# Performance work log

Hardware: AMD Instinct MI355X
Metric: run time of the kernel (lower is better)

The kernel has to match this reference:

```python
import jax, jax.numpy as jnp
import numpy as np

N = 100000   # nodes
E = 1600000  # edges
IN, H1, H2, OUT = 512, 64, 16, 40


def setup_inputs() -> dict:
    key = jax.random.key(0)
    ks = jax.random.split(key, 8)
    x = jax.random.normal(ks[0], (N, IN), jnp.float32)
    edge_index = jax.random.randint(ks[1], (2, E), 0, N, dtype=jnp.int64)

    def glorot(k, i, o):
        s = np.sqrt(6.0 / (i + o)).astype(np.float32)
        return jax.random.uniform(k, (i, o), jnp.float32, -s, s)

    return dict(
        x=x, edge_index=edge_index,
        W1=glorot(ks[2], IN, H1), b1=jnp.zeros((H1,), jnp.float32),
        W2=glorot(ks[3], H1, H2), b2=jnp.zeros((H2,), jnp.float32),
        W3=glorot(ks[4], H2, OUT), b3=jnp.zeros((OUT,), jnp.float32),
    )


def _gcn_conv(x, src, dst, W, b):
    # PyG GCNConv: x' = D^{-1/2} (A + I) D^{-1/2} (x W) + b
    h = x @ W                                   # [N, F_out]
    n = x.shape[0]
    deg = jnp.zeros((n,), h.dtype).at[dst].add(1.0) + 1.0   # self-loop adds 1
    dinv = jax.lax.rsqrt(deg)                   # deg >= 1 always
    norm = dinv[src] * dinv[dst]                # [E]
    msg = h[src] * norm[:, None]                # gather + scale  [E, F_out]
    out = jnp.zeros_like(h).at[dst].add(msg)    # scatter-add to targets
    out = out + h * (dinv * dinv)[:, None]      # self-loop contribution
    return out + b


def reference(x, edge_index, W1, b1, W2, b2, W3, b3):
    src, dst = edge_index[0], edge_index[1]
    h = jax.nn.relu(_gcn_conv(x, src, dst, W1, b1))
    # dropout(p=0.2, training=False) -> identity
    h = jax.nn.relu(_gcn_conv(h, src, dst, W2, b2))
    h = _gcn_conv(h, src, dst, W3, b3)
    return jax.nn.log_softmax(h, axis=-1)
```

## Files before the change

kernel.cpp:

```cpp
#include <hip/hip_runtime.h>
#include <cstdint>
#include <cstddef>

#define NNODES 100000
#define NEDGES 1600000
#define NWIN 100
#define WIN_NODES 1000
#define WCAP 17408
#define WSTR 16

#define GM_ROWS 128
#define APAD 72
#define GEMM_BLOCKS ((NNODES + GM_ROWS - 1) / GM_ROWS)
#define BUCKET_BLOCKS 512
#define BCHUNK ((NEDGES + BUCKET_BLOCKS - 1) / BUCKET_BLOCKS)
#define MEGA_BLOCKS (GEMM_BLOCKS + BUCKET_BLOCKS)

typedef __attribute__((ext_vector_type(8))) short bf16x8;
typedef __attribute__((ext_vector_type(4))) float f32x4;

__device__ inline unsigned short f2bf(float f) {
    union { float f; unsigned u; } v; v.f = f;
    unsigned r = v.u + 0x7FFFu + ((v.u >> 16) & 1u);
    return (unsigned short)(r >> 16);
}
__device__ inline void bfpair(unsigned u, float& lo, float& hi) {
    union { unsigned x; float f; } a, b;
    a.x = u << 16; b.x = u & 0xffff0000u;
    lo = a.f; hi = b.f;
}


__global__ __launch_bounds__(256) void convW(const float* __restrict__ W,
                                             unsigned short* __restrict__ Wt,
                                             int* __restrict__ wcur) {
    if (blockIdx.x == 0 && threadIdx.x < NWIN) wcur[threadIdx.x * WSTR] = 0;
    int i = blockIdx.x * 256 + threadIdx.x;
    if (i < 512 * 64) {
        int k = i >> 6, n = i & 63;
        Wt[n * 512 + k] = f2bf(W[i]);
    }
}


__global__ __launch_bounds__(256) void mega_gemm_bucket(
        const float* __restrict__ A,
        const unsigned short* __restrict__ Wt,
        unsigned short* __restrict__ Hs,
        const int* __restrict__ src, const int* __restrict__ dst,
        unsigned* __restrict__ stage,
        int* __restrict__ wcur, int M, int E) {
    __shared__ __align__(16) unsigned char smem[4 * 32 * APAD * 2];

    long long b = blockIdx.x;
    int g0 = (int)((b * GEMM_BLOCKS) / MEGA_BLOCKS);
    int g1 = (int)(((b + 1) * GEMM_BLOCKS) / MEGA_BLOCKS);

    if (g1 > g0) {
        typedef unsigned short Slice[32][APAD];
        Slice* As = (Slice*)smem;
        const int tid = threadIdx.x;
        const int wv = tid >> 6;
        const int lane = tid & 63;
        const int lm = lane & 15;
        const int lk = (lane >> 4) * 8;
        const int lr4 = lane >> 4;
        const int lc4 = lane & 15;
        const int bm = g0 * GM_ROWS + wv * 32;

        f32x4 acc[2][4];
#pragma unroll
        for (int i = 0; i < 2; i++)
#pragma unroll
            for (int j = 0; j < 4; j++) acc[i][j] = (f32x4){0.f, 0.f, 0.f, 0.f};

        for (int k0 = 0; k0 < 512; k0 += 64) {
#pragma unroll
            for (int p = 0; p < 8; p++) {
                int rl = p * 4 + lr4;
                int row = bm + rl;
                float4 v;
                if (row < M) v = *(const float4*)&A[(size_t)row * 512 + k0 + lc4 * 4];
                else         v = make_float4(0.f, 0.f, 0.f, 0.f);
                unsigned lo, hi;
                asm("v_cvt_pk_bf16_f32 %0, %1, %2" : "=v"(lo) : "v"(v.x), "v"(v.y));
                asm("v_cvt_pk_bf16_f32 %0, %1, %2" : "=v"(hi) : "v"(v.z), "v"(v.w));
                uint2 u; u.x = lo; u.y = hi;
                *(uint2*)&As[wv][rl][lc4 * 4] = u;
            }
            bf16x8 af[2][2];
#pragma unroll
            for (int rf = 0; rf < 2; rf++)
#pragma unroll
                for (int kf = 0; kf < 2; kf++)
                    af[rf][kf] = *(const bf16x8*)&As[wv][rf * 16 + lm][kf * 32 + lk];
            bf16x8 bf[4][2];
#pragma unroll
            for (int cf = 0; cf < 4; cf++)
#pragma unroll
                for (int kf = 0; kf < 2; kf++)
                    bf[cf][kf] = *(const bf16x8*)&Wt[(size_t)(cf * 16 + lm) * 512 + k0 + kf * 32 + lk];

            __builtin_amdgcn_s_setprio(1);
#pragma unroll
            for (int kf = 0; kf < 2; kf++)
#pragma unroll
                for (int rf = 0; rf < 2; rf++)
#pragma unroll
                    for (int cf = 0; cf < 4; cf++)
                        acc[rf][cf] = __builtin_amdgcn_mfma_f32_16x16x32_bf16(
                            af[rf][kf], bf[cf][kf], acc[rf][cf], 0, 0, 0);
            __builtin_amdgcn_s_setprio(0);
        }

#pragma unroll
        for (int rf = 0; rf < 2; rf++) {
#pragma unroll
            for (int j = 0; j < 4; j++) {
                int row = bm + rf * 16 + (lane >> 4) * 4 + j;
                if (row < M) {
#pragma unroll
                    for (int cf = 0; cf < 4; cf++)
                        Hs[(size_t)row * 64 + cf * 16 + lm] = f2bf(acc[rf][cf][j]);
                }
            }
        }
    } else {
        int bi = (int)(b - g0);
        int* cnt  = (int*)smem;
        int* lcur = cnt + NWIN;
        const int tid = threadIdx.x;
        int e0 = bi * BCHUNK;
        int e1 = e0 + BCHUNK; if (e1 > E) e1 = E;

        for (int i = tid; i < NWIN; i += 256) cnt[i] = 0;
        __syncthreads();
        for (int e = e0 + tid; e < e1; e += 256)
            atomicAdd(&cnt[dst[e] / WIN_NODES], 1);
        __syncthreads();
        for (int i = tid; i < NWIN; i += 256)
            lcur[i] = atomicAdd(&wcur[i * WSTR], cnt[i]);
        __syncthreads();
        for (int e = e0 + tid; e < e1; e += 256) {
            int d = dst[e], s = src[e];
            int w = d / WIN_NODES;
            int pos = atomicAdd(&lcur[w], 1);
            if (pos < WCAP)
                stage[(size_t)w * WCAP + pos] =
                    ((unsigned)(d - w * WIN_NODES) << 17) | (unsigned)s;
        }
    }
}


__global__ __launch_bounds__(256) void csr_window(
        const unsigned* __restrict__ stage,
        const int* __restrict__ wcur,
        int* __restrict__ rowstart,
        float* __restrict__ dinv,
        int* __restrict__ csr) {
    __shared__ int cnt[WIN_NODES];
    __shared__ int red[256];
    const int w = blockIdx.x;
    const int t = threadIdx.x;
    const int wb = w * WIN_NODES;
    const size_t sb = (size_t)w * WCAP;

    int v = (t < w) ? min(wcur[t * WSTR], WCAP) : 0;
    red[t] = v;
    __syncthreads();
#pragma unroll
    for (int off = 128; off > 0; off >>= 1) {
        if (t < off) red[t] += red[t + off];
        __syncthreads();
    }
    int woff = red[0];
    int n_w = min(wcur[w * WSTR], WCAP);
    __syncthreads();

    for (int i = t; i < WIN_NODES; i += 256) cnt[i] = 0;
    __syncthreads();
    for (int i = t; i < n_w; i += 256)
        atomicAdd(&cnt[stage[sb + i] >> 17], 1);
    __syncthreads();

    int c0 = 0, c1 = 0, c2 = 0, c3 = 0, psum = 0;
    if (t < 250) {
        c0 = cnt[4 * t]; c1 = cnt[4 * t + 1]; c2 = cnt[4 * t + 2]; c3 = cnt[4 * t + 3];
        psum = c0 + c1 + c2 + c3;
    }
    red[t] = psum;
    __syncthreads();
#pragma unroll
    for (int off = 1; off < 256; off <<= 1) {
        int tv = (t >= off) ? red[t - off] : 0;
        __syncthreads();
        red[t] += tv;
        __syncthreads();
    }
    int excl = red[t] - psum;
    if (t < 250) {
        int running = woff + excl;
        int idx = 4 * t;
        rowstart[wb + idx] = running; dinv[wb + idx] = rsqrtf((float)c0 + 1.f);
        cnt[idx] = running; running += c0;
        rowstart[wb + idx + 1] = running; dinv[wb + idx + 1] = rsqrtf((float)c1 + 1.f);
        cnt[idx + 1] = running; running += c1;
        rowstart[wb + idx + 2] = running; dinv[wb + idx + 2] = rsqrtf((float)c2 + 1.f);
        cnt[idx + 2] = running; running += c2;
        rowstart[wb + idx + 3] = running; dinv[wb + idx + 3] = rsqrtf((float)c3 + 1.f);
        cnt[idx + 3] = running;
    }
    if (w == NWIN - 1 && t == 0) rowstart[NNODES] = woff + n_w;
    __syncthreads();

    for (int i = t; i < n_w; i += 256) {
        unsigned p = stage[sb + i];
        int dl = (int)(p >> 17);
        int s  = (int)(p & 0x1FFFFu);
        int pos = atomicAdd(&cnt[dl], 1);
        csr[pos] = s;
    }
}


__global__ __launch_bounds__(256) void gather64_l2(
        const int* __restrict__ rowstart, const int* __restrict__ csr,
        const float* __restrict__ dinv,
        const unsigned short* __restrict__ Hs1,
        const float* __restrict__ b1,
        const float* __restrict__ W2,
        unsigned short* __restrict__ Hs2,
        int M) {
    __shared__ float Ws2[64 * 16];
    __shared__ float b1s[64];
    __shared__ float srow[8][64];
    for (int i = threadIdx.x; i < 64 * 16; i += 256) Ws2[i] = W2[i];
    if (threadIdx.x < 64) b1s[threadIdx.x] = b1[threadIdx.x];
    __syncthreads();

    const int r = threadIdx.x >> 5;
    const int lf = threadIdx.x & 31;
    const int row = blockIdx.x * 8 + r;
    const bool rok = (row < M);

    float v0 = 0.f, v1 = 0.f;
    if (rok) {
        const unsigned* H32 = (const unsigned*)Hs1;
        int e0 = rowstart[row], e1 = rowstart[row + 1];
        float dd = dinv[row];
        float acc0, acc1;
        bfpair(H32[(size_t)row * 32 + lf], acc0, acc1);
        acc0 *= dd; acc1 *= dd;
        int e = e0;
        for (; e + 3 < e1; e += 4) {
            int s0 = csr[e], s1 = csr[e + 1], s2 = csr[e + 2], s3 = csr[e + 3];
            float w0 = dinv[s0], w1 = dinv[s1], w2 = dinv[s2], w3 = dinv[s3];
            unsigned u0 = H32[(size_t)s0 * 32 + lf];
            unsigned u1 = H32[(size_t)s1 * 32 + lf];
            unsigned u2 = H32[(size_t)s2 * 32 + lf];
            unsigned u3 = H32[(size_t)s3 * 32 + lf];
            float a, b;
            bfpair(u0, a, b); acc0 += w0 * a; acc1 += w0 * b;
            bfpair(u1, a, b); acc0 += w1 * a; acc1 += w1 * b;
            bfpair(u2, a, b); acc0 += w2 * a; acc1 += w2 * b;
            bfpair(u3, a, b); acc0 += w3 * a; acc1 += w3 * b;
        }
        for (; e < e1; e++) {
            int s0 = csr[e];
            float w0 = dinv[s0];
            unsigned u = H32[(size_t)s0 * 32 + lf];
            float a, b;
            bfpair(u, a, b); acc0 += w0 * a; acc1 += w0 * b;
        }
        v0 = fmaxf(acc0 * dd + b1s[2 * lf], 0.f);
        v1 = fmaxf(acc1 * dd + b1s[2 * lf + 1], 0.f);
    }
    float2 t2; t2.x = v0; t2.y = v1;
    *(float2*)&srow[r][2 * lf] = t2;
    __syncthreads();

    if (rok && lf < 16) {
        float acc = 0.f;
#pragma unroll
        for (int k4 = 0; k4 < 16; k4++) {
            float4 s4 = *(const float4*)&srow[r][k4 * 4];
            acc += s4.x * Ws2[(k4 * 4 + 0) * 16 + lf];
            acc += s4.y * Ws2[(k4 * 4 + 1) * 16 + lf];
            acc += s4.z * Ws2[(k4 * 4 + 2) * 16 + lf];
            acc += s4.w * Ws2[(k4 * 4 + 3) * 16 + lf];
        }
        acc *= dinv[row];
        float hi = __shfl_down(acc, 1, 64);
        if ((lf & 1) == 0) {
            unsigned p = (unsigned)f2bf(acc) | ((unsigned)f2bf(hi) << 16);
            ((unsigned*)Hs2)[(size_t)row * 8 + (lf >> 1)] = p;
        }
    }
}


template <int F, bool RELU, bool SCALEOUT, bool HASBIAS, bool OUTBF>
__global__ __launch_bounds__(256) void gather_bf(
        const int* __restrict__ rowstart,
        const int* __restrict__ csr,
        const float* __restrict__ dinv,
        const unsigned short* __restrict__ Hs,
        const float* __restrict__ bias,
        void* __restrict__ outp,
        int M) {
    constexpr int LANES = F / 2;
    constexpr int GP = 256 / LANES;
    int row = blockIdx.x * GP + threadIdx.x / LANES;
    int lf = threadIdx.x % LANES;
    if (row >= M) return;

    const unsigned* H32 = (const unsigned*)Hs;
    const size_t LP = F / 2;

    int e0 = rowstart[row], e1 = rowstart[row + 1];
    float acc0, acc1;
    bfpair(H32[(size_t)row * LP + lf], acc0, acc1);

    int e = e0;
    for (; e + 3 < e1; e += 4) {
        int s0 = csr[e], s1 = csr[e + 1], s2 = csr[e + 2], s3 = csr[e + 3];
        unsigned u0 = H32[(size_t)s0 * LP + lf];
        unsigned u1 = H32[(size_t)s1 * LP + lf];
        unsigned u2 = H32[(size_t)s2 * LP + lf];
        unsigned u3 = H32[(size_t)s3 * LP + lf];
        float a, b;
        bfpair(u0, a, b); acc0 += a; acc1 += b;
        bfpair(u1, a, b); acc0 += a; acc1 += b;
        bfpair(u2, a, b); acc0 += a; acc1 += b;
        bfpair(u3, a, b); acc0 += a; acc1 += b;
    }
    for (; e < e1; e++) {
        unsigned u = H32[(size_t)csr[e] * LP + lf];
        float a, b;
        bfpair(u, a, b); acc0 += a; acc1 += b;
    }

    float dd = dinv[row];
    float v0 = acc0 * dd, v1 = acc1 * dd;
    if (HASBIAS) { v0 += bias[2 * lf]; v1 += bias[2 * lf + 1]; }
    if (RELU) { v0 = fmaxf(v0, 0.f); v1 = fmaxf(v1, 0.f); }
    if (SCALEOUT) { v0 *= dd; v1 *= dd; }
    if (OUTBF) {
        unsigned p = (unsigned)f2bf(v0) | ((unsigned)f2bf(v1) << 16);
        ((unsigned*)outp)[(size_t)row * LP + lf] = p;
    } else {
        float2 t; t.x = v0; t.y = v1;
        ((float2*)outp)[(size_t)row * LP + lf] = t;
    }
}


#define SRP 20

__global__ __launch_bounds__(256) void gather16_final(
        const int* __restrict__ rowstart, const int* __restrict__ csr,
        const float* __restrict__ dinv,
        const unsigned short* __restrict__ r2s,
        const float* __restrict__ W3,
        const float* __restrict__ b3,
        float* __restrict__ out,
        int M) {
    __shared__ float Ws3[16 * 40];
    __shared__ float bs3[40];
    __shared__ float srow[32][SRP];
    __shared__ float orow[32 * 40];
    for (int i = threadIdx.x; i < 16 * 40; i += 256) Ws3[i] = W3[i];
    if (threadIdx.x < 40) bs3[threadIdx.x] = b3[threadIdx.x];

    const int r = threadIdx.x >> 3;
    const int lf = threadIdx.x & 7;
    const int row = blockIdx.x * 32 + r;
    const bool rok = (row < M);

    float g0 = 0.f, g1 = 0.f;
    if (rok) {
        const unsigned* H32 = (const unsigned*)r2s;
        int e0 = rowstart[row], e1 = rowstart[row + 1];
        float acc0, acc1;
        bfpair(H32[(size_t)row * 8 + lf], acc0, acc1);
        int e = e0;
        for (; e + 3 < e1; e += 4) {
            int s0 = csr[e], s1 = csr[e + 1], s2 = csr[e + 2], s3 = csr[e + 3];
            unsigned u0 = H32[(size_t)s0 * 8 + lf];
            unsigned u1 = H32[(size_t)s1 * 8 + lf];
            unsigned u2 = H32[(size_t)s2 * 8 + lf];
            unsigned u3 = H32[(size_t)s3 * 8 + lf];
            float a, b;
            bfpair(u0, a, b); acc0 += a; acc1 += b;
            bfpair(u1, a, b); acc0 += a; acc1 += b;
            bfpair(u2, a, b); acc0 += a; acc1 += b;
            bfpair(u3, a, b); acc0 += a; acc1 += b;
        }
        for (; e < e1; e++) {
            unsigned u = H32[(size_t)csr[e] * 8 + lf];
            float a, b;
            bfpair(u, a, b); acc0 += a; acc1 += b;
        }
        float dd = dinv[row];
        g0 = acc0 * dd; g1 = acc1 * dd;
    }
    float2 t2; t2.x = g0; t2.y = g1;
    *(float2*)&srow[r][2 * lf] = t2;
    __syncthreads();

    float vals[5];
#pragma unroll
    for (int q = 0; q < 5; q++) vals[q] = bs3[lf + 8 * q];
#pragma unroll
    for (int k4 = 0; k4 < 4; k4++) {
        float4 s4 = *(const float4*)&srow[r][k4 * 4];
#pragma unroll
        for (int q = 0; q < 5; q++) {
            int n = lf + 8 * q;
            vals[q] += s4.x * Ws3[(k4 * 4 + 0) * 40 + n];
            vals[q] += s4.y * Ws3[(k4 * 4 + 1) * 40 + n];
            vals[q] += s4.z * Ws3[(k4 * 4 + 2) * 40 + n];
            vals[q] += s4.w * Ws3[(k4 * 4 + 3) * 40 + n];
        }
    }
    float m = vals[0];
#pragma unroll
    for (int q = 1; q < 5; q++) m = fmaxf(m, vals[q]);
#pragma unroll
    for (int off = 1; off < 8; off <<= 1) m = fmaxf(m, __shfl_xor(m, off, 64));
    float s = 0.f;
#pragma unroll
    for (int q = 0; q < 5; q++) s += expf(vals[q] - m);
#pragma unroll
    for (int off = 1; off < 8; off <<= 1) s += __shfl_xor(s, off, 64);
    float ls = logf(s) + m;
#pragma unroll
    for (int q = 0; q < 5; q++) orow[r * 40 + lf + 8 * q] = vals[q] - ls;
    __syncthreads();

    float4* o4 = (float4*)(out + (size_t)blockIdx.x * 32 * 40);
    const float4* s4p = (const float4*)orow;
    for (int i = threadIdx.x; i < 320; i += 256) {
        int rr = (i * 4) / 40;
        if (blockIdx.x * 32 + rr < M) o4[i] = s4p[i];
    }
}


extern "C" void kernel_launch(void* const* d_in, const int* in_sizes, int n_in,
                              void* d_out, int out_size, void* d_ws, size_t ws_size,
                              hipStream_t stream) {
    const float* x   = (const float*)d_in[0];
    const int*   ei  = (const int*)d_in[1];
    const int*   src = ei;
    const int*   dst = ei + NEDGES;
    const float* W1 = (const float*)d_in[2];
    const float* b1 = (const float*)d_in[3];
    const float* W2 = (const float*)d_in[4];
    const float* b2 = (const float*)d_in[5];
    const float* W3 = (const float*)d_in[6];
    const float* b3 = (const float*)d_in[7];
    float* out = (float*)d_out;

    int* ws_i = (int*)d_ws;
    int* wcur     = ws_i;
    int* rowstart = wcur + NWIN * WSTR + 16;
    int* csr      = rowstart + NNODES + 8;
    unsigned* stage = (unsigned*)(csr + NEDGES);
    float* dinv   = (float*)(stage + (size_t)NWIN * WCAP);
    unsigned short* Wt = (unsigned short*)(dinv + NNODES);
    float* bufA   = (float*)((int*)(Wt + 64 * 512) + 16);
    float* bufB   = bufA + (size_t)NNODES * 64;

    unsigned short* Hs1 = (unsigned short*)bufA;
    unsigned short* Hs2 = (unsigned short*)bufB;
    unsigned short* r2s = (unsigned short*)bufA;

    convW<<<128, 256, 0, stream>>>(W1, Wt, wcur);

    mega_gemm_bucket<<<MEGA_BLOCKS, 256, 0, stream>>>(
        x, Wt, Hs1, src, dst, stage, wcur, NNODES, NEDGES);

    csr_window<<<NWIN, 256, 0, stream>>>(stage, wcur, rowstart, dinv, csr);

    gather64_l2<<<(NNODES + 7) / 8, 256, 0, stream>>>(
        rowstart, csr, dinv, Hs1, b1, W2, Hs2, NNODES);

    gather_bf<16, true, true, true, true><<<(NNODES + 31) / 32, 256, 0, stream>>>(
        rowstart, csr, dinv, Hs2, b2, r2s, NNODES);

    gather16_final<<<(NNODES + 31) / 32, 256, 0, stream>>>(
        rowstart, csr, dinv, r2s, W3, b3, out, NNODES);
}
```

Baseline: 231.5 us.

## Double-buffer A tiles via direct global-to-LDS loads with swizzled layout

The first-layer GEMM now streams fp32 A tiles straight into LDS with global_load_lds, double-buffered so the next k-slice loads while the current one is converted to bf16 and fed to MFMA. The LDS layout is XOR-swizzled to avoid bank conflicts, and rows per block drop from 128 to 64, so each wave handles 16 rows and more GEMM blocks run. The goal is to hide the memory latency of reading the large x matrix. The cost is bf16 conversion after the LDS read, more frequent reloading of W per row, and manual vmcnt waits that have to match the number of loads in flight.

```diff
diff --git a/kernel.cpp b/kernel.cpp
--- a/kernel.cpp
+++ b/kernel.cpp
@@ -9,8 +9,7 @@
 #define WCAP 17408
 #define WSTR 16
 
-#define GM_ROWS 128
-#define APAD 72
+#define GM_ROWS 64
 #define GEMM_BLOCKS ((NNODES + GM_ROWS - 1) / GM_ROWS)
 #define BUCKET_BLOCKS 512
 #define BCHUNK ((NEDGES + BUCKET_BLOCKS - 1) / BUCKET_BLOCKS)
@@ -29,6 +28,11 @@
     a.x = u << 16; b.x = u & 0xffff0000u;
     lo = a.f; hi = b.f;
 }
+
+#define GLOAD_LDS16(gp, lp)                                                        \
+    __builtin_amdgcn_global_load_lds(                                              \
+        (__attribute__((address_space(1))) const void*)(gp),                       \
+        (__attribute__((address_space(3))) void*)(lp), 16, 0, 0)
 
 
 __global__ __launch_bounds__(256) void convW(const float* __restrict__ W,
@@ -50,79 +54,92 @@
         const int* __restrict__ src, const int* __restrict__ dst,
         unsigned* __restrict__ stage,
         int* __restrict__ wcur, int M, int E) {
-    __shared__ __align__(16) unsigned char smem[4 * 32 * APAD * 2];
+    __shared__ __align__(16) char smem[32768];
 
     long long b = blockIdx.x;
     int g0 = (int)((b * GEMM_BLOCKS) / MEGA_BLOCKS);
     int g1 = (int)(((b + 1) * GEMM_BLOCKS) / MEGA_BLOCKS);
 
     if (g1 > g0) {
-        typedef unsigned short Slice[32][APAD];
-        Slice* As = (Slice*)smem;
         const int tid = threadIdx.x;
         const int wv = tid >> 6;
         const int lane = tid & 63;
         const int lm = lane & 15;
-        const int lk = (lane >> 4) * 8;
-        const int lr4 = lane >> 4;
-        const int lc4 = lane & 15;
-        const int bm = g0 * GM_ROWS + wv * 32;
-
-        f32x4 acc[2][4];
-#pragma unroll
-        for (int i = 0; i < 2; i++)
-#pragma unroll
-            for (int j = 0; j < 4; j++) acc[i][j] = (f32x4){0.f, 0.f, 0.f, 0.f};
-
-        for (int k0 = 0; k0 < 512; k0 += 64) {
-#pragma unroll
-            for (int p = 0; p < 8; p++) {
-                int rl = p * 4 + lr4;
-                int row = bm + rl;
-                float4 v;
-                if (row < M) v = *(const float4*)&A[(size_t)row * 512 + k0 + lc4 * 4];
-                else         v = make_float4(0.f, 0.f, 0.f, 0.f);
-                unsigned lo, hi;
-                asm("v_cvt_pk_bf16_f32 %0, %1, %2" : "=v"(lo) : "v"(v.x), "v"(v.y));
-                asm("v_cvt_pk_bf16_f32 %0, %1, %2" : "=v"(hi) : "v"(v.z), "v"(v.w));
-                uint2 u; u.x = lo; u.y = hi;
-                *(uint2*)&As[wv][rl][lc4 * 4] = u;
+        const int lk8 = (lane >> 4);
+        const int bm = g0 * GM_ROWS;
+        const int wbase = bm + wv * 16;
+
+        f32x4 acc[4];
+#pragma unroll
+        for (int j = 0; j < 4; j++) acc[j] = (f32x4){0.f, 0.f, 0.f, 0.f};
+
+        const int st_rl = lane >> 4;
+        const int st_u = lane & 15;
+
+        auto ISSUE_A = [&](int k0, int bsel) {
+#pragma unroll
+            for (int i = 0; i < 4; i++) {
+                int rl = 4 * i + st_rl;
+                int grow = wbase + rl;
+                grow = min(grow, M - 1);
+                int su = st_u ^ rl;
+                const float* gp = A + (size_t)grow * 512 + k0 + su * 4;
+                char* lp = smem + bsel * 16384 + wv * 4096 + i * 1024;
+                GLOAD_LDS16(gp, lp);
             }
-            bf16x8 af[2][2];
-#pragma unroll
-            for (int rf = 0; rf < 2; rf++)
+        };
+
+        ISSUE_A(0, 0);
+        for (int t = 0; t < 8; t++) {
+            const int k0 = t * 64;
+            const int bsel = t & 1;
+
+            bf16x8 bb[4][2];
+#pragma unroll
+            for (int cf = 0; cf < 4; cf++)
 #pragma unroll
                 for (int kf = 0; kf < 2; kf++)
-                    af[rf][kf] = *(const bf16x8*)&As[wv][rf * 16 + lm][kf * 32 + lk];
-            bf16x8 bf[4][2];
-#pragma unroll
-            for (int cf = 0; cf < 4; cf++)
-#pragma unroll
-                for (int kf = 0; kf < 2; kf++)
-                    bf[cf][kf] = *(const bf16x8*)&Wt[(size_t)(cf * 16 + lm) * 512 + k0 + kf * 32 + lk];
+                    bb[cf][kf] = *(const bf16x8*)&Wt[(size_t)(cf * 16 + lm) * 512
+                                                     + k0 + kf * 32 + lk8 * 8];
+
+            if (t < 7) ISSUE_A(k0 + 64, bsel ^ 1);
+
+            if (t < 7) { asm volatile("s_waitcnt vmcnt(4)" ::: "memory"); }
+            else       { asm volatile("s_waitcnt vmcnt(0)" ::: "memory"); }
+            __builtin_amdgcn_sched_barrier(0);
+
+            bf16x8 af[2];
+#pragma unroll
+            for (int kf = 0; kf < 2; kf++) {
+                int u0 = kf * 8 + (lk8 << 1);
+                const char* base = smem + bsel * 16384 + wv * 4096 + lm * 256;
+                float4 lo = *(const float4*)(base + (((u0)     ^ lm) << 4));
+                float4 hi = *(const float4*)(base + (((u0 + 1) ^ lm) << 4));
+                unsigned c[4];
+                asm("v_cvt_pk_bf16_f32 %0, %1, %2" : "=v"(c[0]) : "v"(lo.x), "v"(lo.y));
+                asm("v_cvt_pk_bf16_f32 %0, %1, %2" : "=v"(c[1]) : "v"(lo.z), "v"(lo.w));
+                asm("v_cvt_pk_bf16_f32 %0, %1, %2" : "=v"(c[2]) : "v"(hi.x), "v"(hi.y));
+                asm("v_cvt_pk_bf16_f32 %0, %1, %2" : "=v"(c[3]) : "v"(hi.z), "v"(hi.w));
+                af[kf] = *(bf16x8*)c;
+            }
 
             __builtin_amdgcn_s_setprio(1);
 #pragma unroll
             for (int kf = 0; kf < 2; kf++)
 #pragma unroll
-                for (int rf = 0; rf < 2; rf++)
-#pragma unroll
-                    for (int cf = 0; cf < 4; cf++)
-                        acc[rf][cf] = __builtin_amdgcn_mfma_f32_16x16x32_bf16(
-                            af[rf][kf], bf[cf][kf], acc[rf][cf], 0, 0, 0);
+                for (int cf = 0; cf < 4; cf++)
+                    acc[cf] = __builtin_amdgcn_mfma_f32_16x16x32_bf16(
+                        af[kf], bb[cf][kf], acc[cf], 0, 0, 0);
             __builtin_amdgcn_s_setprio(0);
         }
 
 #pragma unroll
-        for (int rf = 0; rf < 2; rf++) {
-#pragma unroll
-            for (int j = 0; j < 4; j++) {
-                int row = bm + rf * 16 + (lane >> 4) * 4 + j;
-                if (row < M) {
-#pragma unroll
-                    for (int cf = 0; cf < 4; cf++)
-                        Hs[(size_t)row * 64 + cf * 16 + lm] = f2bf(acc[rf][cf][j]);
-                }
+        for (int j = 0; j < 4; j++) {
+            int row = wbase + (lane >> 4) * 4 + j;
+            if (row < M) {
+#pragma unroll
+                for (int cf = 0; cf < 4; cf++)
+                    Hs[(size_t)row * 64 + cf * 16 + lm] = f2bf(acc[cf][j]);
             }
         }
     } else {
```

New measurement: 226.5 us. 1.02x faster.
